# Kernel optimization log

Measured on AMD Instinct MI355X. Metric: run time of the kernel, lower is better.

The kernel has to match this reference:

```python
import jax, jax.numpy as jnp
import numpy as np

B, S, D, H = 2, 4096, 512, 8
HD = D // H


def setup_inputs() -> dict:
    key = jax.random.key(0)
    ks = jax.random.split(key, 9)
    scale = 1.0 / np.sqrt(D)
    inp = {
        "x": jax.random.normal(ks[0], (B, S, D), dtype=jnp.float32),
        "Wq": jax.random.normal(ks[1], (D, D), dtype=jnp.float32) * scale,
        "bq": jnp.zeros((D,), dtype=jnp.float32),
        "Wk": jax.random.normal(ks[2], (D, D), dtype=jnp.float32) * scale,
        "bk": jnp.zeros((D,), dtype=jnp.float32),
        "Wv": jax.random.normal(ks[3], (D, D), dtype=jnp.float32) * scale,
        "bv": jnp.zeros((D,), dtype=jnp.float32),
        "Wo": jax.random.normal(ks[4], (D, D), dtype=jnp.float32) * scale,
        "bo": jnp.zeros((D,), dtype=jnp.float32),
    }
    return inp


def reference(x, Wq, bq, Wk, bk, Wv, bv, Wo, bo):
    b, s, d = x.shape
    # projections: nn.Linear computes x @ W.T + b; here W is stored as [d_in, d_out]
    q = x @ Wq + bq
    k = x @ Wk + bk
    v = x @ Wv + bv
    # split heads: [b, s, h*hd] -> [b, h, s, hd]
    def split(t):
        return t.reshape(b, s, H, HD).transpose(0, 2, 1, 3)
    q, k, v = split(q), split(k), split(v)
    att = jnp.einsum('bhil,bhjl->bhij', q, k) / np.sqrt(HD)
    # causal mask
    causal = jnp.tril(jnp.ones((s, s), dtype=bool))
    att = jnp.where(causal[None, None], att, -jnp.inf)
    att = jax.nn.softmax(att, axis=-1)
    out = jnp.einsum('bhil,bhlj->bhij', att, v)  # [b, h, s, hd]
    out = out.transpose(0, 2, 1, 3).reshape(b, s, d)
    out = out @ Wo + bo
    return out
```

## Files before the change

### kernel.cpp

```cpp
#include <hip/hip_runtime.h>
#include <math.h>

#define SS 4096
#define DD 512
#define HH 8
#define QKSCALE 0.1803368801111137f

typedef __attribute__((ext_vector_type(8))) short bf16x8;
typedef __attribute__((ext_vector_type(4))) float f32x4;
typedef __attribute__((ext_vector_type(16))) float f32x16;
typedef __attribute__((ext_vector_type(4))) unsigned int u32x4;

__device__ __forceinline__ void gl2lds16(const void* g, void* l) {
    __builtin_amdgcn_global_load_lds(
        (const __attribute__((address_space(1))) unsigned int*)(uintptr_t)g,
        (__attribute__((address_space(3))) unsigned int*)(uintptr_t)l,
        16, 0, 0);
}

__device__ __forceinline__ unsigned short f2bf(float f) {
    unsigned u = __float_as_uint(f);
    u += 0x7FFF + ((u >> 16) & 1);
    return (unsigned short)(u >> 16);
}

__device__ __forceinline__ unsigned pk_bf(float lo, float hi) {
    unsigned ul = __float_as_uint(lo) + 0x8000u;
    unsigned uh = __float_as_uint(hi) + 0x8000u;
    return __builtin_amdgcn_perm(uh, ul, 0x07060302u);
}

__device__ __forceinline__ float2 upk_bf(unsigned u) {
    float2 r;
    r.x = __uint_as_float(u << 16);
    r.y = __uint_as_float(u & 0xFFFF0000u);
    return r;
}

__global__ __launch_bounds__(256) void cast_x_kernel(const float* __restrict__ x,
                                                     unsigned short* __restrict__ xb) {
    int i = (blockIdx.x * 256 + threadIdx.x) * 4;
    float4 v = *(const float4*)&x[i];
    ushort4 o;
    o.x = f2bf(v.x); o.y = f2bf(v.y); o.z = f2bf(v.z); o.w = f2bf(v.w);
    *(ushort4*)&xb[i] = o;
}

__global__ __launch_bounds__(256) void castT_w_kernel(const float* __restrict__ Wq,
                                                      const float* __restrict__ Wk,
                                                      const float* __restrict__ Wv,
                                                      const float* __restrict__ Wo,
                                                      unsigned short* __restrict__ Wt) {
    const int z = blockIdx.z;
    const float* W = z == 0 ? Wq : z == 1 ? Wk : z == 2 ? Wv : Wo;
    const float scale = (z == 0) ? QKSCALE : 1.0f;
    unsigned short* dst = Wt + (size_t)z * DD * DD;
    __shared__ unsigned short T[64 * 80];
    const int k0 = blockIdx.x * 64, n0 = blockIdx.y * 64;
    const int t = threadIdx.x;
    #pragma unroll
    for (int it = 0; it < 4; it++) {
        int i = t + it * 256;
        int kr = i >> 4, nc = (i & 15) * 4;
        float4 v = *(const float4*)&W[(size_t)(k0 + kr) * DD + n0 + nc];
        T[(nc + 0) * 80 + kr] = f2bf(v.x * scale);
        T[(nc + 1) * 80 + kr] = f2bf(v.y * scale);
        T[(nc + 2) * 80 + kr] = f2bf(v.z * scale);
        T[(nc + 3) * 80 + kr] = f2bf(v.w * scale);
    }
    __syncthreads();
    #pragma unroll
    for (int it = 0; it < 2; it++) {
        int i = t + it * 256;
        int nr = i >> 3, kc = (i & 7) * 8;
        bf16x8 v = *(const bf16x8*)&T[nr * 80 + kc];
        *(bf16x8*)&dst[(size_t)(n0 + nr) * DD + k0 + kc] = v;
    }
}

__global__ __launch_bounds__(256) void v_transpose_kernel(const unsigned short* __restrict__ V,
                                                          unsigned short* __restrict__ Vt) {
    const int s0 = blockIdx.x * 64;
    const int bh = blockIdx.y;
    __shared__ unsigned short T[64 * 80];
    const int t = threadIdx.x;
    const unsigned short* Vg = V + (size_t)bh * SS * 64;
    #pragma unroll
    for (int it = 0; it < 2; it++) {
        int i = t + it * 256;
        int sr = i >> 3, dc = (i & 7) * 8;
        bf16x8 v = *(const bf16x8*)&Vg[(size_t)(s0 + sr) * 64 + dc];
        #pragma unroll
        for (int j = 0; j < 8; j++) T[(dc + j) * 80 + sr] = (unsigned short)v[j];
    }
    __syncthreads();
    unsigned short* Vtg = Vt + (size_t)bh * 64 * SS;
    #pragma unroll
    for (int it = 0; it < 2; it++) {
        int i = t + it * 256;
        int dr = i >> 3, sc = (i & 7) * 8;
        bf16x8 v = *(const bf16x8*)&T[dr * 80 + sc];
        *(bf16x8*)&Vtg[(size_t)dr * SS + s0 + sc] = v;
    }
}

template <int MODE>
__global__ __launch_bounds__(256) void gemm128(const unsigned short* __restrict__ A,
                                               const unsigned short* __restrict__ WtAll,
                                               const float* __restrict__ b0,
                                               const float* __restrict__ b1,
                                               const float* __restrict__ b2,
                                               void* __restrict__ out) {
    const int tid = threadIdx.x;
    const int wave = tid >> 6, lane = tid & 63;
    const int quad = lane >> 4, l16 = lane & 15;
    const int wm = wave >> 1, wn = wave & 1;
    const int bm0 = blockIdx.x * 128;
    const int n_tot = blockIdx.y * 128;
    const int z = (MODE == 0) ? (n_tot >> 9) : 3;
    const int bn0 = (MODE == 0) ? (n_tot & 511) : n_tot;

    const unsigned short* Bt = (MODE == 0) ? (WtAll + (size_t)n_tot * DD)
                                           : (WtAll + (size_t)3 * DD * DD + (size_t)bn0 * DD);

    __shared__ unsigned short As[128 * 64];
    __shared__ unsigned short Bs[128 * 64];

    f32x4 acc[4][4] = {};

    const int lr = lane >> 3;
    const int cpp = lane & 7;

    for (int k0 = 0; k0 < DD; k0 += 64) {
        __syncthreads();
        #pragma unroll
        for (int t = 0; t < 4; t++) {
            int r0 = wave * 32 + t * 8;
            int m = r0 + lr;
            if (MODE == 0) {
                gl2lds16(&A[(size_t)(bm0 + m) * DD + k0 + ((cpp ^ (m & 7)) << 3)], &As[r0 * 64]);
            } else {
                int gm = bm0 + m;
                gl2lds16(&A[((size_t)((gm >> 12) * HH + (k0 >> 6)) * SS + (gm & (SS - 1))) * 64
                            + ((cpp ^ (m & 7)) << 3)], &As[r0 * 64]);
            }
            gl2lds16(&Bt[(size_t)m * DD + k0 + ((cpp ^ (m & 7)) << 3)], &Bs[r0 * 64]);
        }
        __syncthreads();
        #pragma unroll
        for (int kk = 0; kk < 2; kk++) {
            bf16x8 af[4], bf[4];
            #pragma unroll
            for (int mf = 0; mf < 4; mf++) {
                int m = wm * 64 + mf * 16 + l16;
                af[mf] = *(const bf16x8*)&As[m * 64 + (((kk * 4 + quad) ^ (m & 7)) << 3)];
            }
            #pragma unroll
            for (int nf = 0; nf < 4; nf++) {
                int n = wn * 64 + nf * 16 + l16;
                bf[nf] = *(const bf16x8*)&Bs[n * 64 + (((kk * 4 + quad) ^ (n & 7)) << 3)];
            }
            #pragma unroll
            for (int mf = 0; mf < 4; mf++)
                #pragma unroll
                for (int nf = 0; nf < 4; nf++)
                    acc[mf][nf] = __builtin_amdgcn_mfma_f32_16x16x32_bf16(af[mf], bf[nf], acc[mf][nf], 0, 0, 0);
        }
    }

    const float bscale = (MODE == 0 && z == 0) ? QKSCALE : 1.0f;
    const float* bias = (MODE == 0) ? (z == 0 ? b0 : z == 1 ? b1 : b2) : b0;
    #pragma unroll
    for (int nf = 0; nf < 4; nf++) {
        int n = bn0 + wn * 64 + nf * 16 + l16;
        float bv = bias[n] * bscale;
        #pragma unroll
        for (int mf = 0; mf < 4; mf++) {
            #pragma unroll
            for (int r = 0; r < 4; r++) {
                int m = bm0 + wm * 64 + mf * 16 + quad * 4 + r;
                float val = acc[mf][nf][r] + bv;
                if (MODE == 0) {
                    int b = m >> 12, s = m & (SS - 1);
                    int h = n >> 6, d = n & 63;
                    unsigned short* dst = (unsigned short*)out + (size_t)z * 4194304;
                    dst[(((size_t)(b * HH + h)) * SS + s) * 64 + d] = f2bf(val);
                } else {
                    ((float*)out)[(size_t)m * DD + n] = val;
                }
            }
        }
    }
}

__global__ __launch_bounds__(256, 3) void attn_chunk(const unsigned short* __restrict__ Q,
                                                     const unsigned short* __restrict__ K,
                                                     const unsigned short* __restrict__ Vt,
                                                     unsigned short* __restrict__ P0,
                                                     unsigned short* __restrict__ P1,
                                                     unsigned short* __restrict__ P2,
                                                     float* __restrict__ Lpart) {
    const int id = 79 - (int)blockIdx.x;
    int g, base0;
    if (id < 8)       { g = 0; base0 = 0; }
    else if (id < 24) { g = 1; base0 = 8; }
    else if (id < 48) { g = 2; base0 = 24; }
    else              { g = 3; base0 = 48; }
    const int nc = g + 1;
    const int t0 = id - base0;
    const int qt = 8 * g + t0 / nc;
    const int c  = t0 % nc;
    const int nk = 2 * qt + 2;
    const int bsz = nk / nc, rem = nk % nc;
    const int ks = c * bsz + (c < rem ? c : rem);
    const int nit = bsz + (c < rem ? 1 : 0);

    const int bh = blockIdx.y;
    const int tid = threadIdx.x;
    const int wave = tid >> 6, lane = tid & 63;
    const int h = lane >> 5, l31 = lane & 31;
    const int lr = lane >> 3, cpp = lane & 7;

    __shared__ unsigned short sb[16384];
    unsigned short* Ksb0 = sb;
    unsigned short* Ksb1 = sb + 4096;
    unsigned short* Vsb0 = sb + 8192;
    unsigned short* Vsb1 = sb + 12288;

    const unsigned short* Qg = Q + (size_t)bh * SS * 64;
    const unsigned short* Kg = K + (size_t)bh * SS * 64;
    const unsigned short* Vtg = Vt + (size_t)bh * 64 * SS;

    const int q0w = qt * 128 + wave * 32;
    const int qrow = q0w + l31;
    const int qmaxw = q0w + 31;

    bf16x8 qf[4];
    #pragma unroll
    for (int cc = 0; cc < 4; cc++)
        qf[cc] = *(const bf16x8*)&Qg[(size_t)qrow * 64 + cc * 16 + h * 8];

    bf16x8 onesA;
    #pragma unroll
    for (int j = 0; j < 8; j++) onesA[j] = (short)0x3F80;

    f32x16 fz;
    #pragma unroll
    for (int i = 0; i < 16; i++) fz[i] = 0.f;

    f32x16 oacc[2]; oacc[0] = fz; oacc[1] = fz;
    f32x16 lacc = fz;

    #pragma unroll
    for (int t = 0; t < 2; t++) {
        int r0 = wave * 16 + t * 8;
        int m = r0 + lr;
        gl2lds16(&Kg[(size_t)(ks * 64 + m) * 64 + ((cpp ^ (m & 7)) << 3)], &Ksb0[r0 * 64]);
        gl2lds16(&Vtg[(size_t)m * SS + ks * 64 + ((cpp ^ (m & 7)) << 3)], &Vsb0[r0 * 64]);
    }

    for (int it = 0; it < nit; it++) {
        const int kt = ks + it;
        __syncthreads();
        if (it + 1 < nit) {
            unsigned short* Kn = ((it + 1) & 1) ? Ksb1 : Ksb0;
            unsigned short* Vn = ((it + 1) & 1) ? Vsb1 : Vsb0;
            #pragma unroll
            for (int t = 0; t < 2; t++) {
                int r0 = wave * 16 + t * 8;
                int m = r0 + lr;
                gl2lds16(&Kg[(size_t)((kt + 1) * 64 + m) * 64 + ((cpp ^ (m & 7)) << 3)], &Kn[r0 * 64]);
                gl2lds16(&Vtg[(size_t)m * SS + (kt + 1) * 64 + ((cpp ^ (m & 7)) << 3)], &Vn[r0 * 64]);
            }
        }
        if (kt * 64 > qmaxw) continue;

        const unsigned short* Kb = (it & 1) ? Ksb1 : Ksb0;
        const unsigned short* Vb = (it & 1) ? Vsb1 : Vsb0;

        f32x16 sc0 = fz, sc1 = fz;
        #pragma unroll
        for (int cc = 0; cc < 4; cc++) {
            bf16x8 k0 = *(const bf16x8*)&Kb[(0 * 32 + l31) * 64 + (((2 * cc + h) ^ (l31 & 7)) << 3)];
            bf16x8 k1 = *(const bf16x8*)&Kb[(1 * 32 + l31) * 64 + (((2 * cc + h) ^ (l31 & 7)) << 3)];
            sc0 = __builtin_amdgcn_mfma_f32_32x32x16_bf16(k0, qf[cc], sc0, 0, 0, 0);
            sc1 = __builtin_amdgcn_mfma_f32_32x32x16_bf16(k1, qf[cc], sc1, 0, 0, 0);
        }

        if (kt * 64 + 63 > q0w) {
            #pragma unroll
            for (int r = 0; r < 16; r++) {
                int rm = (r & 3) + 8 * (r >> 2) + 4 * h;
                if (kt * 64 + rm > qrow) sc0[r] = -INFINITY;
                if (kt * 64 + 32 + rm > qrow) sc1[r] = -INFINITY;
            }
        }

        unsigned pk[2][4][2];
        #pragma unroll
        for (int b = 0; b < 4; b++)
            #pragma unroll
            for (int pr = 0; pr < 2; pr++) {
                int r = 4 * b + 2 * pr;
                pk[0][b][pr] = pk_bf(__builtin_amdgcn_exp2f(sc0[r]), __builtin_amdgcn_exp2f(sc0[r + 1]));
                pk[1][b][pr] = pk_bf(__builtin_amdgcn_exp2f(sc1[r]), __builtin_amdgcn_exp2f(sc1[r + 1]));
            }

        #pragma unroll
        for (int jt = 0; jt < 4; jt++) {
            const int kh = jt >> 1, be = 2 * (jt & 1);
            unsigned own0 = h ? pk[kh][be + 1][0] : pk[kh][be][0];
            unsigned own1 = h ? pk[kh][be + 1][1] : pk[kh][be][1];
            unsigned snd0 = h ? pk[kh][be][0] : pk[kh][be + 1][0];
            unsigned snd1 = h ? pk[kh][be][1] : pk[kh][be + 1][1];
            unsigned rc0 = (unsigned)__shfl_xor((int)snd0, 32);
            unsigned rc1 = (unsigned)__shfl_xor((int)snd1, 32);
            u32x4 pw;
            pw[0] = h ? rc0 : own0;
            pw[1] = h ? rc1 : own1;
            pw[2] = h ? own0 : rc0;
            pw[3] = h ? own1 : rc1;
            bf16x8 pf = __builtin_bit_cast(bf16x8, pw);
            #pragma unroll
            for (int dh = 0; dh < 2; dh++) {
                bf16x8 vfr = *(const bf16x8*)&Vb[(dh * 32 + l31) * 64 + (((2 * jt + h) ^ (l31 & 7)) << 3)];
                oacc[dh] = __builtin_amdgcn_mfma_f32_32x32x16_bf16(vfr, pf, oacc[dh], 0, 0, 0);
            }
            lacc = __builtin_amdgcn_mfma_f32_32x32x16_bf16(onesA, pf, lacc, 0, 0, 0);
        }
    }

    __syncthreads();
    float* ob = (float*)sb;
    const int q = wave * 32 + l31;
    #pragma unroll
    for (int dh = 0; dh < 2; dh++)
        #pragma unroll
        for (int b = 0; b < 4; b++) {
            int d4 = 2 * b + h + 8 * dh;
            float4 v4;
            v4.x = oacc[dh][4 * b + 0];
            v4.y = oacc[dh][4 * b + 1];
            v4.z = oacc[dh][4 * b + 2];
            v4.w = oacc[dh][4 * b + 3];
            *(float4*)&ob[q * 64 + ((d4 ^ (l31 & 15)) << 2)] = v4;
        }
    if (h == 0) Lpart[((size_t)id * 16 + bh) * 128 + q] = lacc[0];
    __syncthreads();
    unsigned short* Og = (id < 32 ? P0 + (size_t)id * 131072
                        : id < 64 ? P1 + (size_t)(id - 32) * 131072
                                  : P2 + (size_t)(id - 64) * 131072) + (size_t)bh * 8192;
    #pragma unroll
    for (int it = 0; it < 4; it++) {
        int flat = it * 256 + tid;
        int qq = flat >> 3, d8 = flat & 7;
        float4 a = *(const float4*)&ob[qq * 64 + (((d8 * 2) ^ (qq & 15)) << 2)];
        float4 b = *(const float4*)&ob[qq * 64 + (((d8 * 2 + 1) ^ (qq & 15)) << 2)];
        u32x4 o;
        o[0] = pk_bf(a.x, a.y);
        o[1] = pk_bf(a.z, a.w);
        o[2] = pk_bf(b.x, b.y);
        o[3] = pk_bf(b.z, b.w);
        *(u32x4*)&Og[qq * 64 + d8 * 8] = o;
    }
}

__global__ __launch_bounds__(256) void reduce_o(const unsigned short* __restrict__ P0,
                                                const unsigned short* __restrict__ P1,
                                                const unsigned short* __restrict__ P2,
                                                const float* __restrict__ Lpart,
                                                unsigned short* __restrict__ Oh) {
    const int qt = blockIdx.x, bh = blockIdx.y;
    const int g = qt >> 3, nc = g + 1;
    const int starts[4] = {0, 8, 24, 48};
    const int qstart = starts[g] + (qt - 8 * g) * nc;
    const int t = threadIdx.x;
    #pragma unroll
    for (int it = 0; it < 4; it++) {
        int flat = it * 256 + t;
        int q = flat >> 3, d8 = flat & 7;
        float s[8] = {};
        float l = 0.f;
        for (int ic = 0; ic < nc; ic++) {
            int idd = qstart + ic;
            const unsigned short* Og = (idd < 32 ? P0 + (size_t)idd * 131072
                                      : idd < 64 ? P1 + (size_t)(idd - 32) * 131072
                                                 : P2 + (size_t)(idd - 64) * 131072) + (size_t)bh * 8192;
            u32x4 u = *(const u32x4*)&Og[q * 64 + d8 * 8];
            #pragma unroll
            for (int j = 0; j < 4; j++) {
                float2 f = upk_bf(u[j]);
                s[2 * j + 0] += f.x;
                s[2 * j + 1] += f.y;
            }
            l += Lpart[((size_t)idd * 16 + bh) * 128 + q];
        }
        float inv = 1.f / l;
        u32x4 o;
        #pragma unroll
        for (int j = 0; j < 4; j++)
            o[j] = pk_bf(s[2 * j] * inv, s[2 * j + 1] * inv);
        *(u32x4*)&Oh[(((size_t)bh * SS) + qt * 128 + q) * 64 + d8 * 8] = o;
    }
}

extern "C" void kernel_launch(void* const* d_in, const int* in_sizes, int n_in,
                              void* d_out, int out_size, void* d_ws, size_t ws_size,
                              hipStream_t stream) {
    const float* x  = (const float*)d_in[0];
    const float* Wq = (const float*)d_in[1];
    const float* bq = (const float*)d_in[2];
    const float* Wk = (const float*)d_in[3];
    const float* bk = (const float*)d_in[4];
    const float* Wv = (const float*)d_in[5];
    const float* bv = (const float*)d_in[6];
    const float* Wo = (const float*)d_in[7];
    const float* bo = (const float*)d_in[8];
    float* out = (float*)d_out;

    unsigned short* xb  = (unsigned short*)d_ws;
    unsigned short* Wt  = xb + 4194304;
    unsigned short* QKV = Wt + 1048576;
    unsigned short* Vw  = QKV + 2 * (size_t)4194304;
    unsigned short* Vtw = QKV + 3 * (size_t)4194304;
    unsigned short* P0  = xb;
    unsigned short* P1  = Vw;
    unsigned short* P2  = (unsigned short*)((char*)d_ws + 44040192);
    float* Lpart = (float*)((char*)d_ws + 44040192 + 4194304);
    unsigned short* Oh  = QKV;

    cast_x_kernel<<<4096, 256, 0, stream>>>(x, xb);
    castT_w_kernel<<<dim3(8, 8, 4), 256, 0, stream>>>(Wq, Wk, Wv, Wo, Wt);
    gemm128<0><<<dim3(64, 12), 256, 0, stream>>>(xb, Wt, bq, bk, bv, QKV);
    v_transpose_kernel<<<dim3(64, 16), 256, 0, stream>>>(Vw, Vtw);
    attn_chunk<<<dim3(80, 16), 256, 0, stream>>>(QKV, QKV + 4194304, Vtw, P0, P1, P2, Lpart);
    reduce_o<<<dim3(32, 16), 256, 0, stream>>>(P0, P1, P2, Lpart, Oh);
    gemm128<1><<<dim3(64, 4), 256, 0, stream>>>(Oh, Wt, bo, nullptr, nullptr, out);
}
```

Measured before the change: 196.9 us.

## Rebalance causal attention chunk split and merge cast kernels into one launch

Causal attention work is split into 90 chunks per head instead of 80, using five query-tile groups with 1 to 5 key-range chunks each. This gives a finer, more even per-block workload for the long causal rows. The x cast and weight transpose-cast kernels are merged into a single prep launch to save one kernel launch. In exchange there are more partial outputs for reduce_o to combine and a larger scratch area, so the Lpart offset is moved further along.

```diff
diff --git a/kernel.cpp b/kernel.cpp
--- a/kernel.cpp
+++ b/kernel.cpp
@@ -37,27 +37,30 @@
     return r;
 }
 
-__global__ __launch_bounds__(256) void cast_x_kernel(const float* __restrict__ x,
-                                                     unsigned short* __restrict__ xb) {
-    int i = (blockIdx.x * 256 + threadIdx.x) * 4;
-    float4 v = *(const float4*)&x[i];
-    ushort4 o;
-    o.x = f2bf(v.x); o.y = f2bf(v.y); o.z = f2bf(v.z); o.w = f2bf(v.w);
-    *(ushort4*)&xb[i] = o;
-}
-
-__global__ __launch_bounds__(256) void castT_w_kernel(const float* __restrict__ Wq,
-                                                      const float* __restrict__ Wk,
-                                                      const float* __restrict__ Wv,
-                                                      const float* __restrict__ Wo,
-                                                      unsigned short* __restrict__ Wt) {
-    const int z = blockIdx.z;
+__global__ __launch_bounds__(256) void prep(const float* __restrict__ x,
+                                            const float* __restrict__ Wq,
+                                            const float* __restrict__ Wk,
+                                            const float* __restrict__ Wv,
+                                            const float* __restrict__ Wo,
+                                            unsigned short* __restrict__ xb,
+                                            unsigned short* __restrict__ Wt) {
+    __shared__ unsigned short T[64 * 80];
+    const int bx = blockIdx.x;
+    const int t = threadIdx.x;
+    if (bx < 4096) {
+        int i = (bx * 256 + t) * 4;
+        float4 v = *(const float4*)&x[i];
+        ushort4 o;
+        o.x = f2bf(v.x); o.y = f2bf(v.y); o.z = f2bf(v.z); o.w = f2bf(v.w);
+        *(ushort4*)&xb[i] = o;
+        return;
+    }
+    const int idx = bx - 4096;
+    const int z = idx >> 6;
+    const int k0 = ((idx >> 3) & 7) * 64, n0 = (idx & 7) * 64;
     const float* W = z == 0 ? Wq : z == 1 ? Wk : z == 2 ? Wv : Wo;
     const float scale = (z == 0) ? QKSCALE : 1.0f;
     unsigned short* dst = Wt + (size_t)z * DD * DD;
-    __shared__ unsigned short T[64 * 80];
-    const int k0 = blockIdx.x * 64, n0 = blockIdx.y * 64;
-    const int t = threadIdx.x;
     #pragma unroll
     for (int it = 0; it < 4; it++) {
         int i = t + it * 256;
@@ -149,7 +152,7 @@
         __syncthreads();
         #pragma unroll
         for (int kk = 0; kk < 2; kk++) {
-            bf16x8 af[4], bf[4];
+            bf16x8 af[4], bfr[4];
             #pragma unroll
             for (int mf = 0; mf < 4; mf++) {
                 int m = wm * 64 + mf * 16 + l16;
@@ -158,13 +161,13 @@
             #pragma unroll
             for (int nf = 0; nf < 4; nf++) {
                 int n = wn * 64 + nf * 16 + l16;
-                bf[nf] = *(const bf16x8*)&Bs[n * 64 + (((kk * 4 + quad) ^ (n & 7)) << 3)];
+                bfr[nf] = *(const bf16x8*)&Bs[n * 64 + (((kk * 4 + quad) ^ (n & 7)) << 3)];
             }
             #pragma unroll
             for (int mf = 0; mf < 4; mf++)
                 #pragma unroll
                 for (int nf = 0; nf < 4; nf++)
-                    acc[mf][nf] = __builtin_amdgcn_mfma_f32_16x16x32_bf16(af[mf], bf[nf], acc[mf][nf], 0, 0, 0);
+                    acc[mf][nf] = __builtin_amdgcn_mfma_f32_16x16x32_bf16(af[mf], bfr[nf], acc[mf][nf], 0, 0, 0);
         }
     }
 
@@ -200,16 +203,14 @@
                                                      unsigned short* __restrict__ P1,
                                                      unsigned short* __restrict__ P2,
                                                      float* __restrict__ Lpart) {
-    const int id = 79 - (int)blockIdx.x;
-    int g, base0;
-    if (id < 8)       { g = 0; base0 = 0; }
-    else if (id < 24) { g = 1; base0 = 8; }
-    else if (id < 48) { g = 2; base0 = 24; }
-    else              { g = 3; base0 = 48; }
-    const int nc = g + 1;
-    const int t0 = id - base0;
-    const int qt = 8 * g + t0 / nc;
-    const int c  = t0 % nc;
+    const int id = 89 - (int)blockIdx.x;
+    int qt, c;
+    if (id < 7)       { qt = id;                 c = 0; }
+    else if (id < 21) { int t = id - 7;  qt = 7 + t / 2;  c = t % 2; }
+    else if (id < 42) { int t = id - 21; qt = 14 + t / 3; c = t % 3; }
+    else if (id < 70) { int t = id - 42; qt = 21 + t / 4; c = t % 4; }
+    else              { int t = id - 70; qt = 28 + t / 5; c = t % 5; }
+    const int nc = (qt < 7) ? 1 : (qt < 14) ? 2 : (qt < 21) ? 3 : (qt < 28) ? 4 : 5;
     const int nk = 2 * qt + 2;
     const int bsz = nk / nc, rem = nk % nc;
     const int ks = c * bsz + (c < rem ? c : rem);
@@ -298,12 +299,12 @@
 
         unsigned pk[2][4][2];
         #pragma unroll
-        for (int b = 0; b < 4; b++)
+        for (int bq = 0; bq < 4; bq++)
             #pragma unroll
             for (int pr = 0; pr < 2; pr++) {
-                int r = 4 * b + 2 * pr;
-                pk[0][b][pr] = pk_bf(__builtin_amdgcn_exp2f(sc0[r]), __builtin_amdgcn_exp2f(sc0[r + 1]));
-                pk[1][b][pr] = pk_bf(__builtin_amdgcn_exp2f(sc1[r]), __builtin_amdgcn_exp2f(sc1[r + 1]));
+                int r = 4 * bq + 2 * pr;
+                pk[0][bq][pr] = pk_bf(__builtin_amdgcn_exp2f(sc0[r]), __builtin_amdgcn_exp2f(sc0[r + 1]));
+                pk[1][bq][pr] = pk_bf(__builtin_amdgcn_exp2f(sc1[r]), __builtin_amdgcn_exp2f(sc1[r + 1]));
             }
 
         #pragma unroll
@@ -336,13 +337,13 @@
     #pragma unroll
     for (int dh = 0; dh < 2; dh++)
         #pragma unroll
-        for (int b = 0; b < 4; b++) {
-            int d4 = 2 * b + h + 8 * dh;
+        for (int bq = 0; bq < 4; bq++) {
+            int d4 = 2 * bq + h + 8 * dh;
             float4 v4;
-            v4.x = oacc[dh][4 * b + 0];
-            v4.y = oacc[dh][4 * b + 1];
-            v4.z = oacc[dh][4 * b + 2];
-            v4.w = oacc[dh][4 * b + 3];
+            v4.x = oacc[dh][4 * bq + 0];
+            v4.y = oacc[dh][4 * bq + 1];
+            v4.z = oacc[dh][4 * bq + 2];
+            v4.w = oacc[dh][4 * bq + 3];
             *(float4*)&ob[q * 64 + ((d4 ^ (l31 & 15)) << 2)] = v4;
         }
     if (h == 0) Lpart[((size_t)id * 16 + bh) * 128 + q] = lacc[0];
@@ -355,12 +356,12 @@
         int flat = it * 256 + tid;
         int qq = flat >> 3, d8 = flat & 7;
         float4 a = *(const float4*)&ob[qq * 64 + (((d8 * 2) ^ (qq & 15)) << 2)];
-        float4 b = *(const float4*)&ob[qq * 64 + (((d8 * 2 + 1) ^ (qq & 15)) << 2)];
+        float4 bb = *(const float4*)&ob[qq * 64 + (((d8 * 2 + 1) ^ (qq & 15)) << 2)];
         u32x4 o;
         o[0] = pk_bf(a.x, a.y);
         o[1] = pk_bf(a.z, a.w);
-        o[2] = pk_bf(b.x, b.y);
-        o[3] = pk_bf(b.z, b.w);
+        o[2] = pk_bf(bb.x, bb.y);
+        o[3] = pk_bf(bb.z, bb.w);
         *(u32x4*)&Og[qq * 64 + d8 * 8] = o;
     }
 }
@@ -371,9 +372,12 @@
                                                 const float* __restrict__ Lpart,
                                                 unsigned short* __restrict__ Oh) {
     const int qt = blockIdx.x, bh = blockIdx.y;
-    const int g = qt >> 3, nc = g + 1;
-    const int starts[4] = {0, 8, 24, 48};
-    const int qstart = starts[g] + (qt - 8 * g) * nc;
+    int nc, qs;
+    if (qt < 7)       { nc = 1; qs = qt; }
+    else if (qt < 14) { nc = 2; qs = 7 + 2 * (qt - 7); }
+    else if (qt < 21) { nc = 3; qs = 21 + 3 * (qt - 14); }
+    else if (qt < 28) { nc = 4; qs = 42 + 4 * (qt - 21); }
+    else              { nc = 5; qs = 70 + 5 * (qt - 28); }
     const int t = threadIdx.x;
     #pragma unroll
     for (int it = 0; it < 4; it++) {
@@ -382,7 +386,7 @@
         float s[8] = {};
         float l = 0.f;
         for (int ic = 0; ic < nc; ic++) {
-            int idd = qstart + ic;
+            int idd = qs + ic;
             const unsigned short* Og = (idd < 32 ? P0 + (size_t)idd * 131072
                                       : idd < 64 ? P1 + (size_t)(idd - 32) * 131072
                                                  : P2 + (size_t)(idd - 64) * 131072) + (size_t)bh * 8192;
@@ -426,14 +430,13 @@
     unsigned short* P0  = xb;
     unsigned short* P1  = Vw;
     unsigned short* P2  = (unsigned short*)((char*)d_ws + 44040192);
-    float* Lpart = (float*)((char*)d_ws + 44040192 + 4194304);
+    float* Lpart = (float*)((char*)d_ws + 44040192 + 6815744);
     unsigned short* Oh  = QKV;
 
-    cast_x_kernel<<<4096, 256, 0, stream>>>(x, xb);
-    castT_w_kernel<<<dim3(8, 8, 4), 256, 0, stream>>>(Wq, Wk, Wv, Wo, Wt);
+    prep<<<4352, 256, 0, stream>>>(x, Wq, Wk, Wv, Wo, xb, Wt);
     gemm128<0><<<dim3(64, 12), 256, 0, stream>>>(xb, Wt, bq, bk, bv, QKV);
     v_transpose_kernel<<<dim3(64, 16), 256, 0, stream>>>(Vw, Vtw);
-    attn_chunk<<<dim3(80, 16), 256, 0, stream>>>(QKV, QKV + 4194304, Vtw, P0, P1, P2, Lpart);
+    attn_chunk<<<dim3(90, 16), 256, 0, stream>>>(QKV, QKV + 4194304, Vtw, P0, P1, P2, Lpart);
     reduce_o<<<dim3(32, 16), 256, 0, stream>>>(P0, P1, P2, Lpart, Oh);
     gemm128<1><<<dim3(64, 4), 256, 0, stream>>>(Oh, Wt, bo, nullptr, nullptr, out);
 }
```

After: 193.3 us. No clear change (-1.8%).
